# Performance work log

Hardware: AMD Instinct MI355X
Metric: run time of the kernel (lower is better)

The kernel has to match this reference:

```python
import jax, jax.numpy as jnp
import numpy as np

N_RAYS = 65536   # 256x256 image
N_PTS = 128      # samples per ray
FEAT = 3         # RGB
FAR_DELTA = 1e10 # sentinel delta for last sample, as in the torch module


def setup_inputs() -> dict:
    key = jax.random.key(0)
    k1, k2, k3 = jax.random.split(key, 3)
    # depths along each ray must be increasing (deltas computed by diff)
    depth_values = jnp.sort(
        jax.random.uniform(k1, (N_RAYS, N_PTS), jnp.float32, 2.0, 6.0), axis=-1)
    density = jax.random.uniform(k2, (N_RAYS, N_PTS), jnp.float32)  # non-negative
    feature = jax.random.uniform(k3, (N_RAYS, N_PTS, FEAT), jnp.float32)
    return {"depth_values": depth_values, "density": density, "feature": feature}


def reference(depth_values, density, feature):
    n_rays, n_pts = depth_values.shape
    # deltas: consecutive depth differences, huge value appended for last bin
    deltas = jnp.concatenate(
        [depth_values[:, 1:] - depth_values[:, :-1],
         jnp.full((n_rays, 1), FAR_DELTA, depth_values.dtype)], axis=-1)
    tau = density * deltas                              # [n_rays, n_pts]
    # transmittance T_i = exp(-sum_{j<i} tau_j) (exclusive cumsum in log space)
    log_T = -jnp.concatenate(
        [jnp.zeros((n_rays, 1), tau.dtype), jnp.cumsum(tau[:, :-1], axis=-1)],
        axis=-1)
    weights = jnp.exp(log_T) * (1.0 - jnp.exp(-tau))    # [n_rays, n_pts]
    feat_out = jnp.einsum('np,npf->nf', weights, feature)         # [n_rays, F]
    depth_out = jnp.sum(weights * depth_values, axis=-1, keepdims=True)
    return jnp.concatenate([feat_out, depth_out], axis=-1)        # [n_rays, F+1]
```

## Files before the change

kernel.cpp:

```cpp
#include <hip/hip_runtime.h>

#define N_RAYS 65536
#define N_PTS 128
#define FEAT 3
#define FAR_DELTA 1e10f

__global__ __launch_bounds__(256) void volrend_kernel(
    const float* __restrict__ depth,
    const float* __restrict__ density,
    const float* __restrict__ feature,
    float* __restrict__ out)
{
    const int wave = threadIdx.x >> 6;
    const int lane = threadIdx.x & 63;
    const int ray  = (blockIdx.x << 2) + wave;

    const int base = ray * N_PTS;
    const float2 d   = *(const float2*)(depth   + base + 2 * lane);
    const float2 rho = *(const float2*)(density + base + 2 * lane);

    float next_dx = __shfl_down(d.x, 1);
    float delta_a = d.y - d.x;
    float delta_b = (lane == 63) ? FAR_DELTA : (next_dx - d.y);

    float tau_a = rho.x * delta_a;
    float tau_b = rho.y * delta_b;
    float pair  = tau_a + tau_b;

    float e = __shfl_up(pair, 1);
    if (lane == 0) e = 0.0f;
    #pragma unroll
    for (int off = 1; off < 64; off <<= 1) {
        float t = __shfl_up(e, off);
        if (lane >= off) e += t;
    }

    float Ta   = __expf(-e);
    float Tmid = __expf(-(e + tau_a));
    float Tend = __expf(-(e + tau_a + tau_b));
    float w_a = Ta - Tmid;
    float w_b = Tmid - Tend;

    const float2* f2 = (const float2*)(feature + (size_t)ray * (N_PTS * FEAT)
                                       + 6 * lane);
    float2 fa = f2[0];
    float2 fb = f2[1];
    float2 fc = f2[2];

    float acc0 = w_a * fa.x + w_b * fb.y;
    float acc1 = w_a * fa.y + w_b * fc.x;
    float acc2 = w_a * fb.x + w_b * fc.y;
    float acc3 = w_a * d.x  + w_b * d.y;

    #pragma unroll
    for (int off = 32; off > 0; off >>= 1) {
        acc0 += __shfl_down(acc0, off);
        acc1 += __shfl_down(acc1, off);
        acc2 += __shfl_down(acc2, off);
        acc3 += __shfl_down(acc3, off);
    }

    if (lane == 0) {
        *(float4*)(out + ray * 4) = make_float4(acc0, acc1, acc2, acc3);
    }
}

extern "C" void kernel_launch(void* const* d_in, const int* in_sizes, int n_in,
                              void* d_out, int out_size, void* d_ws, size_t ws_size,
                              hipStream_t stream) {
    const float* depth   = (const float*)d_in[0];
    const float* density = (const float*)d_in[1];
    const float* feature = (const float*)d_in[2];
    float* out = (float*)d_out;

    dim3 grid(N_RAYS / 4);
    dim3 block(256);
    volrend_kernel<<<grid, block, 0, stream>>>(depth, density, feature, out);
}
```

Measured before the change: 189.1 us.

## Process four rays per wave with half-wave segments and float4 loads

Each wave now handles four rays: two 32-lane segments, each covering two rays, with every lane owning four consecutive samples. Depth, density and feature data are loaded as float4, and the prefix scan and reduction use width-32 shuffles with one fewer step. The grid shrinks fourfold. This is meant to raise memory-level parallelism and cut shuffle and instruction overhead per ray, at the cost of more registers per thread and fewer blocks.

Result: no change. 190.1 us (+0.5%).

```diff
diff --git a/kernel.cpp b/kernel.cpp
--- a/kernel.cpp
+++ b/kernel.cpp
@@ -13,55 +13,83 @@
 {
     const int wave = threadIdx.x >> 6;
     const int lane = threadIdx.x & 63;
-    const int ray  = (blockIdx.x << 2) + wave;
+    const int seg  = lane >> 5;
+    const int s    = lane & 31;
+    const int base = (blockIdx.x * 4 + wave) * 4;
 
-    const int base = ray * N_PTS;
-    const float2 d   = *(const float2*)(depth   + base + 2 * lane);
-    const float2 rho = *(const float2*)(density + base + 2 * lane);
+    const int rayA = base + seg;
+    const int rayB = base + 2 + seg;
 
-    float next_dx = __shfl_down(d.x, 1);
-    float delta_a = d.y - d.x;
-    float delta_b = (lane == 63) ? FAR_DELTA : (next_dx - d.y);
+    const float4 dA = *(const float4*)(depth   + rayA * N_PTS + 4 * s);
+    const float4 rA = *(const float4*)(density + rayA * N_PTS + 4 * s);
+    const float4 dB = *(const float4*)(depth   + rayB * N_PTS + 4 * s);
+    const float4 rB = *(const float4*)(density + rayB * N_PTS + 4 * s);
+    const float4* fA = (const float4*)(feature + (size_t)rayA * (N_PTS * FEAT)) + 3 * s;
+    const float4* fB = (const float4*)(feature + (size_t)rayB * (N_PTS * FEAT)) + 3 * s;
+    const float4 fA0 = fA[0], fA1 = fA[1], fA2 = fA[2];
+    const float4 fB0 = fB[0], fB1 = fB[1], fB2 = fB[2];
 
-    float tau_a = rho.x * delta_a;
-    float tau_b = rho.y * delta_b;
-    float pair  = tau_a + tau_b;
+    float nxA = __shfl_down(dA.x, 1);
+    float nxB = __shfl_down(dB.x, 1);
+    const bool last = (s == 31);
+    float tA0 = rA.x * (dA.y - dA.x);
+    float tA1 = rA.y * (dA.z - dA.y);
+    float tA2 = rA.z * (dA.w - dA.z);
+    float tA3 = rA.w * (last ? FAR_DELTA : (nxA - dA.w));
+    float tB0 = rB.x * (dB.y - dB.x);
+    float tB1 = rB.y * (dB.z - dB.y);
+    float tB2 = rB.z * (dB.w - dB.z);
+    float tB3 = rB.w * (last ? FAR_DELTA : (nxB - dB.w));
 
-    float e = __shfl_up(pair, 1);
-    if (lane == 0) e = 0.0f;
+    float pA = tA0 + tA1 + tA2 + tA3;
+    float pB = tB0 + tB1 + tB2 + tB3;
+    float eA = __shfl_up(pA, 1, 32);
+    float eB = __shfl_up(pB, 1, 32);
+    if (s == 0) { eA = 0.0f; eB = 0.0f; }
     #pragma unroll
-    for (int off = 1; off < 64; off <<= 1) {
-        float t = __shfl_up(e, off);
-        if (lane >= off) e += t;
+    for (int off = 1; off < 32; off <<= 1) {
+        float xA = __shfl_up(eA, off, 32);
+        float xB = __shfl_up(eB, off, 32);
+        if (s >= off) { eA += xA; eB += xB; }
     }
 
-    float Ta   = __expf(-e);
-    float Tmid = __expf(-(e + tau_a));
-    float Tend = __expf(-(e + tau_a + tau_b));
-    float w_a = Ta - Tmid;
-    float w_b = Tmid - Tend;
+    float TA0 = __expf(-eA);
+    float TA1 = __expf(-(eA + tA0));
+    float TA2 = __expf(-(eA + tA0 + tA1));
+    float TA3 = __expf(-(eA + tA0 + tA1 + tA2));
+    float TA4 = __expf(-(eA + pA));
+    float TB0 = __expf(-eB);
+    float TB1 = __expf(-(eB + tB0));
+    float TB2 = __expf(-(eB + tB0 + tB1));
+    float TB3 = __expf(-(eB + tB0 + tB1 + tB2));
+    float TB4 = __expf(-(eB + pB));
+    float wA0 = TA0 - TA1, wA1 = TA1 - TA2, wA2 = TA2 - TA3, wA3 = TA3 - TA4;
+    float wB0 = TB0 - TB1, wB1 = TB1 - TB2, wB2 = TB2 - TB3, wB3 = TB3 - TB4;
 
-    const float2* f2 = (const float2*)(feature + (size_t)ray * (N_PTS * FEAT)
-                                       + 6 * lane);
-    float2 fa = f2[0];
-    float2 fb = f2[1];
-    float2 fc = f2[2];
-
-    float acc0 = w_a * fa.x + w_b * fb.y;
-    float acc1 = w_a * fa.y + w_b * fc.x;
-    float acc2 = w_a * fb.x + w_b * fc.y;
-    float acc3 = w_a * d.x  + w_b * d.y;
+    float a0 = wA0 * fA0.x + wA1 * fA0.w + wA2 * fA1.z + wA3 * fA2.y;
+    float a1 = wA0 * fA0.y + wA1 * fA1.x + wA2 * fA1.w + wA3 * fA2.z;
+    float a2 = wA0 * fA0.z + wA1 * fA1.y + wA2 * fA2.x + wA3 * fA2.w;
+    float a3 = wA0 * dA.x  + wA1 * dA.y  + wA2 * dA.z  + wA3 * dA.w;
+    float b0 = wB0 * fB0.x + wB1 * fB0.w + wB2 * fB1.z + wB3 * fB2.y;
+    float b1 = wB0 * fB0.y + wB1 * fB1.x + wB2 * fB1.w + wB3 * fB2.z;
+    float b2 = wB0 * fB0.z + wB1 * fB1.y + wB2 * fB2.x + wB3 * fB2.w;
+    float b3 = wB0 * dB.x  + wB1 * dB.y  + wB2 * dB.z  + wB3 * dB.w;
 
     #pragma unroll
-    for (int off = 32; off > 0; off >>= 1) {
-        acc0 += __shfl_down(acc0, off);
-        acc1 += __shfl_down(acc1, off);
-        acc2 += __shfl_down(acc2, off);
-        acc3 += __shfl_down(acc3, off);
+    for (int off = 16; off > 0; off >>= 1) {
+        a0 += __shfl_down(a0, off, 32);
+        a1 += __shfl_down(a1, off, 32);
+        a2 += __shfl_down(a2, off, 32);
+        a3 += __shfl_down(a3, off, 32);
+        b0 += __shfl_down(b0, off, 32);
+        b1 += __shfl_down(b1, off, 32);
+        b2 += __shfl_down(b2, off, 32);
+        b3 += __shfl_down(b3, off, 32);
     }
 
-    if (lane == 0) {
-        *(float4*)(out + ray * 4) = make_float4(acc0, acc1, acc2, acc3);
+    if (s == 0) {
+        *(float4*)(out + (size_t)rayA * 4) = make_float4(a0, a1, a2, a3);
+        *(float4*)(out + (size_t)rayB * 4) = make_float4(b0, b1, b2, b3);
     }
 }
 
@@ -73,7 +101,7 @@
     const float* feature = (const float*)d_in[2];
     float* out = (float*)d_out;
 
-    dim3 grid(N_RAYS / 4);
+    dim3 grid(N_RAYS / 16);
     dim3 block(256);
     volrend_kernel<<<grid, block, 0, stream>>>(depth, density, feature, out);
 }
```
